# Performance work log

Measured on AMD Instinct MI355X. Metric: run time of the kernel, lower is better.

## Reference

```python
import math
import jax, jax.numpy as jnp
import numpy as np

DIM = 1024
N_HEADS = 16
HEAD_DIM = DIM // N_HEADS
SEQ_LEN = 2048
BASE = 10000.0
EPS = 1e-5


def rope_cache(seq_len, dim):
    pos = jnp.arange(seq_len, dtype=jnp.float32)[:, None]          # (S,1)
    di = jnp.arange(0, dim, 2, dtype=jnp.float32) / dim            # (d/2,)
    theta = pos * jnp.exp(-di * math.log(BASE))                    # (S,d/2)
    cos = jnp.repeat(jnp.cos(theta), 2, axis=1)                    # (S,d)
    sin = jnp.repeat(jnp.sin(theta), 2, axis=1)
    return cos, sin


def rotate_half(x):
    # NOTE: faithful to source: concatenate (-odd, even), not interleave
    x1 = x[..., ::2]
    x2 = x[..., 1::2]
    return jnp.concatenate((-x2, x1), axis=-1)


def layernorm(x, gamma, beta):
    mu = jnp.mean(x, axis=-1, keepdims=True)
    var = jnp.var(x, axis=-1, keepdims=True)
    return (x - mu) * jax.lax.rsqrt(var + EPS) * gamma + beta


def setup_inputs() -> dict:
    key = jax.random.key(0)
    ks = jax.random.split(key, 7)
    s = 1.0 / math.sqrt(DIM)
    return {
        "x": jax.random.normal(ks[0], (2, SEQ_LEN, DIM), dtype=jnp.float32),
        "Wq": jax.random.normal(ks[1], (DIM, DIM), dtype=jnp.float32) * s,
        "Wk": jax.random.normal(ks[2], (DIM, DIM), dtype=jnp.float32) * s,
        "Wv": jax.random.normal(ks[3], (DIM, DIM), dtype=jnp.float32) * s,
        "q_gamma": jnp.ones((HEAD_DIM,), jnp.float32),
        "q_beta": jnp.zeros((HEAD_DIM,), jnp.float32),
        "k_gamma": jnp.ones((HEAD_DIM,), jnp.float32),
        "k_beta": jnp.zeros((HEAD_DIM,), jnp.float32),
        "Wo": jax.random.normal(ks[4], (DIM, DIM), dtype=jnp.float32) * s,
        "bo": jnp.zeros((DIM,), jnp.float32),
    }


def reference(x, Wq, Wk, Wv, q_gamma, q_beta, k_gamma, k_beta, Wo, bo):
    B, S, D = x.shape
    H, hd = N_HEADS, HEAD_DIM
    # QKV projections (torch Linear: x @ W.T)
    q = (x @ Wq.T).reshape(B, S, H, hd).transpose(0, 2, 1, 3)  # (B,H,S,hd)
    k = (x @ Wk.T).reshape(B, S, H, hd).transpose(0, 2, 1, 3)
    v = (x @ Wv.T).reshape(B, S, H, hd).transpose(0, 2, 1, 3)
    # QK-norm over head_dim
    q = layernorm(q, q_gamma, q_beta)
    k = layernorm(k, k_gamma, k_beta)
    # RoPE
    cos, sin = rope_cache(S, hd)  # (S,hd)
    cos = cos[None, None]
    sin = sin[None, None]
    q = q * cos + rotate_half(q) * sin
    k = k * cos + rotate_half(k) * sin
    # causal attention
    scale = 1.0 / math.sqrt(hd)
    scores = scale * jnp.einsum('bhqd,bhkd->bhqk', q, k)
    mask = jnp.tril(jnp.ones((S, S), dtype=bool))
    scores = jnp.where(mask, scores, -jnp.inf)
    attn = jax.nn.softmax(scores, axis=-1)
    out = jnp.einsum('bhqk,bhkd->bhqd', attn, v)
    out = out.transpose(0, 2, 1, 3).reshape(B, S, D)
    return out @ Wo.T + bo
```

## Files before the change

kernel.cpp:

```cpp
#include <hip/hip_runtime.h>
#include <hip/hip_bf16.h>

#define SEQ   2048
#define NH    16
#define HD    64
#define BATCH 2
#define DIMM  1024

typedef __attribute__((ext_vector_type(8))) __bf16 bfrag;
typedef __attribute__((ext_vector_type(4))) float f32x4;

__device__ __forceinline__ short f2b(float f) {
  unsigned x = __float_as_uint(f);
  x += 0x7fff + ((x >> 16) & 1);
  return (short)(x >> 16);
}
__device__ __forceinline__ float b2f(short s) {
  unsigned u = ((unsigned)(unsigned short)s) << 16;
  return __uint_as_float(u);
}
__device__ __forceinline__ short f2b_pk(float f) {
  unsigned r;
  asm("v_cvt_pk_bf16_f32 %0, %1, %1" : "=v"(r) : "v"(f));
  return (short)r;
}

__device__ __forceinline__ void gload16(const void* g, void* l) {
  __builtin_amdgcn_global_load_lds(
      (const __attribute__((address_space(1))) void*)g,
      (__attribute__((address_space(3))) void*)l, 16, 0, 0);
}

__global__ __launch_bounds__(256) void k_prep(
    const float* __restrict__ x, const float* __restrict__ w0,
    const float* __restrict__ w1, const float* __restrict__ w2,
    const float* __restrict__ w3, short* __restrict__ xb,
    short* __restrict__ wb, float* __restrict__ cstab) {
  int b = blockIdx.x;
  if (b < 4096) {
    int i = b * 256 + threadIdx.x;
    float4 v = reinterpret_cast<const float4*>(x)[i];
    short4 o;
    o.x = f2b(v.x); o.y = f2b(v.y); o.z = f2b(v.z); o.w = f2b(v.w);
    reinterpret_cast<short4*>(xb)[i] = o;
  } else if (b < 8192) {
    int bb = b - 4096;
    int widx = bb >> 10;
    const float* src = widx == 0 ? w0 : (widx == 1 ? w1 : (widx == 2 ? w2 : w3));
    int i = (bb & 1023) * 256 + threadIdx.x;
    float4 v = reinterpret_cast<const float4*>(src)[i];
    short4 o;
    o.x = f2b(v.x); o.y = f2b(v.y); o.z = f2b(v.z); o.w = f2b(v.w);
    reinterpret_cast<short4*>(wb + (size_t)widx * 1048576)[i] = o;
  } else {
    int gid = (b - 8192) * 256 + threadIdx.x;
    int s = gid >> 5, i = gid & 31;
    float freq = expf(-(float)(2 * i) * (1.0f / 64.0f) * 9.210340371976184f);
    float th = (float)s * freq;
    cstab[gid * 2]     = cosf(th);
    cstab[gid * 2 + 1] = sinf(th);
  }
}

__global__ __launch_bounds__(256) void k_gemm_qkv(
    const short* __restrict__ xb, const short* __restrict__ wb,
    short* __restrict__ Qh, short* __restrict__ Kh, short* __restrict__ Vt) {
  __shared__ alignas(16) short As[128 * 64];
  __shared__ alignas(16) short Bs[128 * 64];
  const int tid = threadIdx.x;
  const int lane = tid & 63, w = tid >> 6;
  const int wr = w >> 1, wc = w & 1;
  const int bm = blockIdx.x, bn = blockIdx.y;
  const int widx = bn >> 3;
  const int brow0 = (bn & 7) * 128;
  const short* Wp = wb + (size_t)widx * (1 << 20);

  const int l15 = lane & 15, lq = lane >> 4, l7 = lane & 7;
  const int srow = lane >> 3;
  const int sslot = l7 ^ srow;

  f32x4 acc[4][4] = {};

  for (int kk = 0; kk < 1024; kk += 64) {
#pragma unroll
    for (int p = 0; p < 4; ++p) {
      int rr = p * 32 + w * 8 + srow;
      gload16(&xb[(size_t)(bm * 128 + rr) * 1024 + kk + sslot * 8],
              &As[p * 2048 + w * 512]);
      gload16(&Wp[(size_t)(brow0 + rr) * 1024 + kk + sslot * 8],
              &Bs[p * 2048 + w * 512]);
    }
    __syncthreads();
#pragma unroll
    for (int ks = 0; ks < 2; ++ks) {
      bfrag af[4], bf[4];
      int slot = (ks * 4 + lq) ^ l7;
#pragma unroll
      for (int mi = 0; mi < 4; ++mi)
        af[mi] = *(const bfrag*)&As[(wr * 64 + mi * 16 + l15) * 64 + slot * 8];
#pragma unroll
      for (int ni = 0; ni < 4; ++ni)
        bf[ni] = *(const bfrag*)&Bs[(wc * 64 + ni * 16 + l15) * 64 + slot * 8];
#pragma unroll
      for (int mi = 0; mi < 4; ++mi)
#pragma unroll
        for (int ni = 0; ni < 4; ++ni)
          acc[mi][ni] = __builtin_amdgcn_mfma_f32_16x16x32_bf16(af[mi], bf[ni], acc[mi][ni], 0, 0, 0);
    }
    __syncthreads();
  }

  if (widx < 2) {
    short* dst = widx == 0 ? Qh : Kh;
#pragma unroll
    for (int mi = 0; mi < 4; ++mi) {
#pragma unroll
      for (int ni = 0; ni < 4; ++ni) {
        int ng = bn * 128 + wc * 64 + ni * 16 + l15;
        int col = ng & 1023, h = col >> 6, d = col & 63;
#pragma unroll
        for (int r = 0; r < 4; ++r) {
          int mg = bm * 128 + wr * 64 + mi * 16 + lq * 4 + r;
          int b = mg >> 11, s = mg & 2047;
          dst[((size_t)((b * 16 + h) * 2048 + s)) * 64 + d] = f2b(acc[mi][ni][r]);
        }
      }
    }
  } else {
#pragma unroll
    for (int mi = 0; mi < 4; ++mi) {
#pragma unroll
      for (int ni = 0; ni < 4; ++ni) {
        int ng = bn * 128 + wc * 64 + ni * 16 + l15;
        int col = ng & 1023, h = col >> 6, d = col & 63;
        int mg0 = bm * 128 + wr * 64 + mi * 16 + lq * 4;
        int b = mg0 >> 11, s0 = mg0 & 2047;
        short4 sv;
        sv.x = f2b(acc[mi][ni][0]); sv.y = f2b(acc[mi][ni][1]);
        sv.z = f2b(acc[mi][ni][2]); sv.w = f2b(acc[mi][ni][3]);
        *reinterpret_cast<short4*>(
            &Vt[((size_t)((b * 16 + h) * 64 + d)) * 2048 + s0]) = sv;
      }
    }
  }
}

__global__ __launch_bounds__(256) void k_ln_rope(
    short* __restrict__ Qh, short* __restrict__ Kh,
    const float* __restrict__ qg, const float* __restrict__ qb_,
    const float* __restrict__ kg, const float* __restrict__ kb_,
    const float* __restrict__ cstab) {
  __shared__ float Ysh[32 * 64];
  const int tid = threadIdx.x;
  const int rloc = tid >> 3;
  const int g = tid & 7;
  const int d0 = g * 8;
  const int row = blockIdx.x * 32 + rloc;
  const int which = blockIdx.y;
  short* ptr = which ? Kh : Qh;
  const float* gamma = which ? kg : qg;
  const float* beta  = which ? kb_ : qb_;
  const int s = row & 2047;

  short vs[8];
  *reinterpret_cast<uint4*>(vs) =
      *reinterpret_cast<const uint4*>(&ptr[(size_t)row * 64 + d0]);
  float x[8];
#pragma unroll
  for (int j = 0; j < 8; ++j) x[j] = b2f(vs[j]);
  float s1 = 0.0f, s2 = 0.0f;
#pragma unroll
  for (int j = 0; j < 8; ++j) { s1 += x[j]; s2 = fmaf(x[j], x[j], s2); }
#pragma unroll
  for (int off = 1; off < 8; off <<= 1) {
    s1 += __shfl_xor(s1, off, 8);
    s2 += __shfl_xor(s2, off, 8);
  }
  float mu = s1 * (1.0f / 64.0f);
  float var = s2 * (1.0f / 64.0f) - mu * mu;
  float rs = rsqrtf(var + 1e-5f);

  float gv[8], bv[8];
  *reinterpret_cast<float4*>(&gv[0]) = *reinterpret_cast<const float4*>(&gamma[d0]);
  *reinterpret_cast<float4*>(&gv[4]) = *reinterpret_cast<const float4*>(&gamma[d0 + 4]);
  *reinterpret_cast<float4*>(&bv[0]) = *reinterpret_cast<const float4*>(&beta[d0]);
  *reinterpret_cast<float4*>(&bv[4]) = *reinterpret_cast<const float4*>(&beta[d0 + 4]);
  float y[8];
#pragma unroll
  for (int j = 0; j < 8; ++j) y[j] = (x[j] - mu) * rs * gv[j] + bv[j];

  *reinterpret_cast<float4*>(&Ysh[rloc * 64 + d0])     = *reinterpret_cast<float4*>(&y[0]);
  *reinterpret_cast<float4*>(&Ysh[rloc * 64 + d0 + 4]) = *reinterpret_cast<float4*>(&y[4]);
  __syncthreads();

  float2 cs4[4];
  *reinterpret_cast<float4*>(&cs4[0]) =
      *reinterpret_cast<const float4*>(&cstab[((size_t)s * 32 + g * 4) * 2]);
  *reinterpret_cast<float4*>(&cs4[2]) =
      *reinterpret_cast<const float4*>(&cstab[((size_t)s * 32 + g * 4 + 2) * 2]);

  short o[8];
#pragma unroll
  for (int j = 0; j < 8; ++j) {
    int d = d0 + j;
    float pv = (d < 32) ? Ysh[rloc * 64 + 2 * d + 1]
                        : Ysh[rloc * 64 + 2 * (d - 32)];
    float c = cs4[j >> 1].x, sn = cs4[j >> 1].y;
    float ov = (d < 32) ? (y[j] * c - pv * sn) : (y[j] * c + pv * sn);
    o[j] = f2b_pk(ov);
  }
  *reinterpret_cast<uint4*>(&ptr[(size_t)row * 64 + d0]) =
      *reinterpret_cast<uint4*>(o);
}

__global__ __launch_bounds__(256) void k_attn(
    const short* __restrict__ Qh, const short* __restrict__ Kh,
    const short* __restrict__ Vtg, short* __restrict__ Ob) {
  __shared__ alignas(16) short Ks[2][64 * 64];
  __shared__ alignas(16) short Vs[2][64 * 64];
  __shared__ alignas(16) short Ps[4][16 * 72];
  const int d_ = blockIdx.x;
  const int xcd = d_ & 7, idx = d_ >> 3;
  const int bh = xcd * 4 + (idx >> 4);
  const int pairi = idx & 15;
  const int b = bh >> 4, h = bh & 15;
  const int tid = threadIdx.x, lane = tid & 63, w = tid >> 6;
  const short* Qp = Qh + (size_t)bh * SEQ * 64;
  const short* Kp = Kh + (size_t)bh * SEQ * 64;
  const short* Vp = Vtg + (size_t)bh * 64 * SEQ;

  const int srow = lane >> 3;
  const int sslot = (lane & 7) ^ srow;

  const int l15 = lane & 15;
  const int l7 = lane & 7;
  const int lq = lane >> 4;

  auto STAGE = [&](int buf, int kb) {
#pragma unroll
    for (int j = 0; j < 2; ++j) {
      int rr = w * 16 + j * 8 + srow;
      gload16(&Kp[(size_t)(kb * 64 + rr) * 64 + sslot * 8],
              &Ks[buf][w * 1024 + j * 512]);
      gload16(&Vp[(size_t)rr * 2048 + kb * 64 + sslot * 8],
              &Vs[buf][w * 1024 + j * 512]);
    }
  };

#pragma unroll 1
  for (int t = 0; t < 2; ++t) {
    const int qt = (t == 0) ? pairi : 31 - pairi;
    const int nkb = qt + 1;

    const int qrow_l = qt * 64 + w * 16 + l15;
    bfrag qf[2];
#pragma unroll
    for (int c = 0; c < 2; ++c)
      qf[c] = *(const bfrag*)&Qp[(size_t)qrow_l * 64 + c * 32 + lq * 8];

    f32x4 oacc[4] = {};
    float lrow[4] = {0.0f, 0.0f, 0.0f, 0.0f};

    STAGE(0, 0);
    __syncthreads();

    int cur = 0;
#pragma unroll 1
    for (int kb = 0; kb < nkb; ++kb) {
      if (kb + 1 < nkb) STAGE(cur ^ 1, kb + 1);

      f32x4 sacc[4] = {};
      __builtin_amdgcn_s_setprio(1);
#pragma unroll
      for (int c2 = 0; c2 < 4; ++c2) {
        int krow = c2 * 16 + l15;
#pragma unroll
        for (int dc = 0; dc < 2; ++dc) {
          int slot = (dc * 4 + lq) ^ l7;
          bfrag kf = *(const bfrag*)&Ks[cur][krow * 64 + slot * 8];
          sacc[c2] = __builtin_amdgcn_mfma_f32_16x16x32_bf16(qf[dc], kf, sacc[c2], 0, 0, 0);
        }
      }
      __builtin_amdgcn_s_setprio(0);

      const bool diag = (kb == qt);
      const int qg0 = qt * 64 + w * 16 + lq * 4;
#pragma unroll
      for (int r = 0; r < 4; ++r) {
        float pv4[4];
#pragma unroll
        for (int c2 = 0; c2 < 4; ++c2) {
          float s2 = fmaf(sacc[c2][r], 0.18033688011112042f, -11.541560327111707f);
          if (diag && (kb * 64 + c2 * 16 + l15 > qg0 + r)) s2 = -1e30f;
          pv4[c2] = __builtin_amdgcn_exp2f(s2);
        }
        lrow[r] += (pv4[0] + pv4[1]) + (pv4[2] + pv4[3]);
#pragma unroll
        for (int c2 = 0; c2 < 4; ++c2)
          Ps[w][(lq * 4 + r) * 72 + c2 * 16 + l15] = f2b_pk(pv4[c2]);
      }

      bfrag pf[2];
#pragma unroll
      for (int kf2 = 0; kf2 < 2; ++kf2)
        pf[kf2] = *(const bfrag*)&Ps[w][l15 * 72 + kf2 * 32 + lq * 8];
      __builtin_amdgcn_s_setprio(1);
#pragma unroll
      for (int dc = 0; dc < 4; ++dc) {
        int drow = dc * 16 + l15;
#pragma unroll
        for (int kf2 = 0; kf2 < 2; ++kf2) {
          int slot = (kf2 * 4 + lq) ^ l7;
          bfrag vf = *(const bfrag*)&Vs[cur][drow * 64 + slot * 8];
          oacc[dc] = __builtin_amdgcn_mfma_f32_16x16x32_bf16(pf[kf2], vf, oacc[dc], 0, 0, 0);
        }
      }
      __builtin_amdgcn_s_setprio(0);

      __syncthreads();
      cur ^= 1;
    }

    float inv[4];
#pragma unroll
    for (int r = 0; r < 4; ++r) {
#pragma unroll
      for (int off = 1; off < 16; off <<= 1) lrow[r] += __shfl_xor(lrow[r], off);
      inv[r] = 1.0f / lrow[r];
    }
#pragma unroll
    for (int dc = 0; dc < 4; ++dc) {
#pragma unroll
      for (int r = 0; r < 4; ++r) {
        int qg = qt * 64 + w * 16 + lq * 4 + r;
        Ob[(size_t)(b * SEQ + qg) * 1024 + h * 64 + dc * 16 + l15] =
            f2b(oacc[dc][r] * inv[r]);
      }
    }
    __syncthreads();
  }
}

__global__ __launch_bounds__(256) void k_gemm_out(
    const short* __restrict__ Ab, const short* __restrict__ Wp,
    const float* __restrict__ bo, float* __restrict__ out) {
  __shared__ alignas(16) short As[128 * 64];
  __shared__ alignas(16) short Bs[128 * 64];
  const int tid = threadIdx.x;
  const int lane = tid & 63, w = tid >> 6;
  const int wr = w >> 1, wc = w & 1;
  const int bm = blockIdx.x, bn = blockIdx.y;
  const int brow0 = bn * 128;

  const int l15 = lane & 15, lq = lane >> 4, l7 = lane & 7;
  const int srow = lane >> 3;
  const int sslot = l7 ^ srow;

  f32x4 acc[4][4] = {};

  for (int kk = 0; kk < 1024; kk += 64) {
#pragma unroll
    for (int p = 0; p < 4; ++p) {
      int rr = p * 32 + w * 8 + srow;
      gload16(&Ab[(size_t)(bm * 128 + rr) * 1024 + kk + sslot * 8],
              &As[p * 2048 + w * 512]);
      gload16(&Wp[(size_t)(brow0 + rr) * 1024 + kk + sslot * 8],
              &Bs[p * 2048 + w * 512]);
    }
    __syncthreads();
#pragma unroll
    for (int ks = 0; ks < 2; ++ks) {
      bfrag af[4], bf[4];
      int slot = (ks * 4 + lq) ^ l7;
#pragma unroll
      for (int mi = 0; mi < 4; ++mi)
        af[mi] = *(const bfrag*)&As[(wr * 64 + mi * 16 + l15) * 64 + slot * 8];
#pragma unroll
      for (int ni = 0; ni < 4; ++ni)
        bf[ni] = *(const bfrag*)&Bs[(wc * 64 + ni * 16 + l15) * 64 + slot * 8];
#pragma unroll
      for (int mi = 0; mi < 4; ++mi)
#pragma unroll
        for (int ni = 0; ni < 4; ++ni)
          acc[mi][ni] = __builtin_amdgcn_mfma_f32_16x16x32_bf16(af[mi], bf[ni], acc[mi][ni], 0, 0, 0);
    }
    __syncthreads();
  }

#pragma unroll
  for (int mi = 0; mi < 4; ++mi) {
#pragma unroll
    for (int ni = 0; ni < 4; ++ni) {
      int ng = bn * 128 + wc * 64 + ni * 16 + l15;
      float bias = bo[ng];
#pragma unroll
      for (int r = 0; r < 4; ++r) {
        int mg = bm * 128 + wr * 64 + mi * 16 + lq * 4 + r;
        out[(size_t)mg * 1024 + ng] = acc[mi][ni][r] + bias;
      }
    }
  }
}

extern "C" void kernel_launch(void* const* d_in, const int* in_sizes, int n_in,
                              void* d_out, int out_size, void* d_ws, size_t ws_size,
                              hipStream_t stream) {
  const float* x  = (const float*)d_in[0];
  const float* Wq = (const float*)d_in[1];
  const float* Wk = (const float*)d_in[2];
  const float* Wv = (const float*)d_in[3];
  const float* qgamma = (const float*)d_in[4];
  const float* qbeta  = (const float*)d_in[5];
  const float* kgamma = (const float*)d_in[6];
  const float* kbeta  = (const float*)d_in[7];
  const float* Wo = (const float*)d_in[8];
  const float* bo = (const float*)d_in[9];
  float* out = (float*)d_out;

  char* ws = (char*)d_ws;
  short* xb    = (short*)(ws);
  short* wb    = (short*)(ws + 8388608);
  short* Qh    = (short*)(ws + 16777216);
  short* Kh    = (short*)(ws + 25165824);
  short* Vt    = (short*)(ws + 33554432);
  short* Obuf  = (short*)(ws + 41943040);
  float* cstab = (float*)(ws + 50331648);

  k_prep<<<8448, 256, 0, stream>>>(x, Wq, Wk, Wv, Wo, xb, wb, cstab);

  k_gemm_qkv<<<dim3(32, 24), 256, 0, stream>>>(xb, wb, Qh, Kh, Vt);
  k_ln_rope<<<dim3(2048, 2), 256, 0, stream>>>(
      Qh, Kh, qgamma, qbeta, kgamma, kbeta, cstab);
  k_attn<<<512, 256, 0, stream>>>(Qh, Kh, Vt, Obuf);
  k_gemm_out<<<dim3(32, 8), 256, 0, stream>>>(Obuf, wb + 3145728, bo, out);
}
```

Measured before the change: 129.5 us.

## Double-buffer LDS in QKV and output GEMMs and remap blocks per XCD

Both GEMM kernels now use two LDS buffers, so global-to-LDS loads for the next k-tile are issued while MFMAs run on the current tile. This drops one barrier per iteration and hides load latency. The 2D grids become 1D with an index remap that places blocks sharing weight tiles on the same XCD for L2 reuse, and s_setprio raises wave priority around the MFMA bursts. LDS use per block doubles to 64KB, which may lower occupancy.

```diff
diff --git a/kernel.cpp b/kernel.cpp
--- a/kernel.cpp
+++ b/kernel.cpp
@@ -65,12 +65,15 @@
 __global__ __launch_bounds__(256) void k_gemm_qkv(
     const short* __restrict__ xb, const short* __restrict__ wb,
     short* __restrict__ Qh, short* __restrict__ Kh, short* __restrict__ Vt) {
-  __shared__ alignas(16) short As[128 * 64];
-  __shared__ alignas(16) short Bs[128 * 64];
+  __shared__ alignas(16) short As[2][128 * 64];
+  __shared__ alignas(16) short Bs[2][128 * 64];
   const int tid = threadIdx.x;
   const int lane = tid & 63, w = tid >> 6;
   const int wr = w >> 1, wc = w & 1;
-  const int bm = blockIdx.x, bn = blockIdx.y;
+  const int id = blockIdx.x;
+  const int xcd = id & 7, j = id >> 3;
+  const int bn = xcd * 3 + j % 3;
+  const int bm = j / 3;
   const int widx = bn >> 3;
   const int brow0 = (bn & 7) * 128;
   const short* Wp = wb + (size_t)widx * (1 << 20);
@@ -81,33 +84,43 @@
 
   f32x4 acc[4][4] = {};
 
-  for (int kk = 0; kk < 1024; kk += 64) {
+  auto STAGE = [&](int buf, int kk) {
 #pragma unroll
     for (int p = 0; p < 4; ++p) {
       int rr = p * 32 + w * 8 + srow;
       gload16(&xb[(size_t)(bm * 128 + rr) * 1024 + kk + sslot * 8],
-              &As[p * 2048 + w * 512]);
+              &As[buf][p * 2048 + w * 512]);
       gload16(&Wp[(size_t)(brow0 + rr) * 1024 + kk + sslot * 8],
-              &Bs[p * 2048 + w * 512]);
-    }
-    __syncthreads();
+              &Bs[buf][p * 2048 + w * 512]);
+    }
+  };
+
+  STAGE(0, 0);
+  __syncthreads();
+  int cur = 0;
+#pragma unroll 1
+  for (int t = 0; t < 16; ++t) {
+    if (t + 1 < 16) STAGE(cur ^ 1, (t + 1) * 64);
 #pragma unroll
     for (int ks = 0; ks < 2; ++ks) {
       bfrag af[4], bf[4];
       int slot = (ks * 4 + lq) ^ l7;
 #pragma unroll
       for (int mi = 0; mi < 4; ++mi)
-        af[mi] = *(const bfrag*)&As[(wr * 64 + mi * 16 + l15) * 64 + slot * 8];
+        af[mi] = *(const bfrag*)&As[cur][(wr * 64 + mi * 16 + l15) * 64 + slot * 8];
 #pragma unroll
       for (int ni = 0; ni < 4; ++ni)
-        bf[ni] = *(const bfrag*)&Bs[(wc * 64 + ni * 16 + l15) * 64 + slot * 8];
+        bf[ni] = *(const bfrag*)&Bs[cur][(wc * 64 + ni * 16 + l15) * 64 + slot * 8];
+      __builtin_amdgcn_s_setprio(1);
 #pragma unroll
       for (int mi = 0; mi < 4; ++mi)
 #pragma unroll
         for (int ni = 0; ni < 4; ++ni)
           acc[mi][ni] = __builtin_amdgcn_mfma_f32_16x16x32_bf16(af[mi], bf[ni], acc[mi][ni], 0, 0, 0);
+      __builtin_amdgcn_s_setprio(0);
     }
     __syncthreads();
+    cur ^= 1;
   }
 
   if (widx < 2) {
@@ -344,12 +357,13 @@
 __global__ __launch_bounds__(256) void k_gemm_out(
     const short* __restrict__ Ab, const short* __restrict__ Wp,
     const float* __restrict__ bo, float* __restrict__ out) {
-  __shared__ alignas(16) short As[128 * 64];
-  __shared__ alignas(16) short Bs[128 * 64];
+  __shared__ alignas(16) short As[2][128 * 64];
+  __shared__ alignas(16) short Bs[2][128 * 64];
   const int tid = threadIdx.x;
   const int lane = tid & 63, w = tid >> 6;
   const int wr = w >> 1, wc = w & 1;
-  const int bm = blockIdx.x, bn = blockIdx.y;
+  const int id = blockIdx.x;
+  const int bn = id & 7, bm = id >> 3;
   const int brow0 = bn * 128;
 
   const int l15 = lane & 15, lq = lane >> 4, l7 = lane & 7;
@@ -358,33 +372,43 @@
 
   f32x4 acc[4][4] = {};
 
-  for (int kk = 0; kk < 1024; kk += 64) {
+  auto STAGE = [&](int buf, int kk) {
 #pragma unroll
     for (int p = 0; p < 4; ++p) {
       int rr = p * 32 + w * 8 + srow;
       gload16(&Ab[(size_t)(bm * 128 + rr) * 1024 + kk + sslot * 8],
-              &As[p * 2048 + w * 512]);
+              &As[buf][p * 2048 + w * 512]);
       gload16(&Wp[(size_t)(brow0 + rr) * 1024 + kk + sslot * 8],
-              &Bs[p * 2048 + w * 512]);
-    }
-    __syncthreads();
+              &Bs[buf][p * 2048 + w * 512]);
+    }
+  };
+
+  STAGE(0, 0);
+  __syncthreads();
+  int cur = 0;
+#pragma unroll 1
+  for (int t = 0; t < 16; ++t) {
+    if (t + 1 < 16) STAGE(cur ^ 1, (t + 1) * 64);
 #pragma unroll
     for (int ks = 0; ks < 2; ++ks) {
       bfrag af[4], bf[4];
       int slot = (ks * 4 + lq) ^ l7;
 #pragma unroll
       for (int mi = 0; mi < 4; ++mi)
-        af[mi] = *(const bfrag*)&As[(wr * 64 + mi * 16 + l15) * 64 + slot * 8];
+        af[mi] = *(const bfrag*)&As[cur][(wr * 64 + mi * 16 + l15) * 64 + slot * 8];
 #pragma unroll
       for (int ni = 0; ni < 4; ++ni)
-        bf[ni] = *(const bfrag*)&Bs[(wc * 64 + ni * 16 + l15) * 64 + slot * 8];
+        bf[ni] = *(const bfrag*)&Bs[cur][(wc * 64 + ni * 16 + l15) * 64 + slot * 8];
+      __builtin_amdgcn_s_setprio(1);
 #pragma unroll
       for (int mi = 0; mi < 4; ++mi)
 #pragma unroll
         for (int ni = 0; ni < 4; ++ni)
           acc[mi][ni] = __builtin_amdgcn_mfma_f32_16x16x32_bf16(af[mi], bf[ni], acc[mi][ni], 0, 0, 0);
+      __builtin_amdgcn_s_setprio(0);
     }
     __syncthreads();
+    cur ^= 1;
   }
 
 #pragma unroll
@@ -428,9 +452,9 @@
 
   k_prep<<<8448, 256, 0, stream>>>(x, Wq, Wk, Wv, Wo, xb, wb, cstab);
 
-  k_gemm_qkv<<<dim3(32, 24), 256, 0, stream>>>(xb, wb, Qh, Kh, Vt);
+  k_gemm_qkv<<<768, 256, 0, stream>>>(xb, wb, Qh, Kh, Vt);
   k_ln_rope<<<dim3(2048, 2), 256, 0, stream>>>(
       Qh, Kh, qgamma, qbeta, kgamma, kbeta, cstab);
   k_attn<<<512, 256, 0, stream>>>(Qh, Kh, Vt, Obuf);
-  k_gemm_out<<<dim3(32, 8), 256, 0, stream>>>(Obuf, wb + 3145728, bo, out);
-}
+  k_gemm_out<<<256, 256, 0, stream>>>(Obuf, wb + 3145728, bo, out);
+}
```

Result: faster. 126.7 us (-2.1%).
